# Performance work log

Measured on AMD Instinct MI355X. Metric: run time of the kernel, lower is better.

The kernel has to match this reference:

```python
import jax, jax.numpy as jnp
import numpy as np

B, S_IMG, S_TXT = 1, 3072, 512
D_MODEL, H, D_HEAD = 3072, 24, 128
INNER = H * D_HEAD
EPS = 1e-5


def rms_norm(x, w):
    # x: [..., D_HEAD]
    var = jnp.mean(jnp.square(x), axis=-1, keepdims=True)
    return x * jax.lax.rsqrt(var + EPS) * w


def apply_rope(x, cos, sin):
    # x: [B,S,H,D]; cos/sin: [S,D]; interleaved (non-neox) rotation
    x1 = x[..., 0::2]
    x2 = x[..., 1::2]
    rot = jnp.stack([-x2, x1], axis=-1).reshape(x.shape)
    c = cos[None, :, None, :]
    s = sin[None, :, None, :]
    return x * c + rot * s


def setup_inputs() -> dict:
    key = jax.random.key(0)
    ks = jax.random.split(key, 12)
    sc = 1.0 / np.sqrt(D_MODEL)
    ang = jax.random.uniform(ks[10], (S_TXT + S_IMG, D_HEAD), jnp.float32, 0.0, 2 * np.pi)
    return {
        "hidden_states": jax.random.normal(ks[0], (B, S_IMG, D_MODEL), jnp.float32),
        "encoder_hidden_states": jax.random.normal(ks[1], (B, S_TXT, D_MODEL), jnp.float32),
        "cos": jnp.cos(ang),
        "sin": jnp.sin(ang),
        "W_qkv": jax.random.normal(ks[2], (3 * INNER, D_MODEL), jnp.float32) * sc,
        "W_add_qkv": jax.random.normal(ks[3], (3 * INNER, D_MODEL), jnp.float32) * sc,
        "b_add_qkv": jnp.zeros((3 * INNER,), jnp.float32),
        "norm_q_w": jnp.ones((D_HEAD,), jnp.float32),
        "norm_k_w": jnp.ones((D_HEAD,), jnp.float32),
        "norm_add_q_w": jnp.ones((D_HEAD,), jnp.float32),
        "norm_add_k_w": jnp.ones((D_HEAD,), jnp.float32),
        "W_out": jax.random.normal(ks[4], (D_MODEL, INNER), jnp.float32) * sc,
        "b_out": jnp.zeros((D_MODEL,), jnp.float32),
        "W_add_out": jax.random.normal(ks[5], (D_MODEL, INNER), jnp.float32) * sc,
        "b_add_out": jnp.zeros((D_MODEL,), jnp.float32),
    }


def reference(hidden_states, encoder_hidden_states, cos, sin,
              W_qkv, W_add_qkv, b_add_qkv,
              norm_q_w, norm_k_w, norm_add_q_w, norm_add_k_w,
              W_out, b_out, W_add_out, b_add_out):
    # fused QKV projections
    qkv = jnp.einsum('bsd,ed->bse', hidden_states, W_qkv)
    q, k, v = jnp.split(qkv, 3, axis=-1)
    eqkv = jnp.einsum('bsd,ed->bse', encoder_hidden_states, W_add_qkv) + b_add_qkv
    eq, ek, ev = jnp.split(eqkv, 3, axis=-1)

    def heads(x):
        return x.reshape(x.shape[0], x.shape[1], H, D_HEAD)

    q, k, v = heads(q), heads(k), heads(v)
    eq, ek, ev = heads(eq), heads(ek), heads(ev)

    # per-head RMSNorm on queries/keys
    q = rms_norm(q, norm_q_w)
    k = rms_norm(k, norm_k_w)
    eq = rms_norm(eq, norm_add_q_w)
    ek = rms_norm(ek, norm_add_k_w)

    # joint concat: text first, then image
    q = jnp.concatenate([eq, q], axis=1)
    k = jnp.concatenate([ek, k], axis=1)
    v = jnp.concatenate([ev, v], axis=1)

    # RoPE on full joint sequence
    q = apply_rope(q, cos, sin)
    k = apply_rope(k, cos, sin)

    # non-causal softmax attention, scale = 1/sqrt(head_dim)
    scale = 1.0 / np.sqrt(D_HEAD)
    scores = jnp.einsum('bqhd,bkhd->bhqk', q, k) * scale
    probs = jax.nn.softmax(scores, axis=-1)
    out = jnp.einsum('bhqk,bkhd->bqhd', probs, v)  # [B,S,H,D]
    out = out.reshape(out.shape[0], out.shape[1], INNER)

    enc_out = out[:, :S_TXT]
    img_out = out[:, S_TXT:]
    enc_out = jnp.einsum('bse,de->bsd', enc_out, W_add_out) + b_add_out
    img_out = jnp.einsum('bse,de->bsd', img_out, W_out) + b_out
    return (img_out, enc_out)
```

## Files before the change

### kernel.cpp

```cpp
#include <hip/hip_runtime.h>


typedef unsigned short u16;
typedef __attribute__((ext_vector_type(2))) unsigned short u16x2;
typedef __attribute__((ext_vector_type(4))) unsigned short u16x4;
typedef __attribute__((ext_vector_type(8))) unsigned short u16x8;
typedef __attribute__((ext_vector_type(8))) short bf16x8;
typedef __attribute__((ext_vector_type(4))) float f32x4;
typedef __attribute__((ext_vector_type(16))) float f32x16;
typedef __attribute__((ext_vector_type(4))) unsigned u32x4;

#define DEV __device__ __forceinline__

DEV u16 f2bf(float f) {
  unsigned u = __builtin_bit_cast(unsigned, f);
  u = (u + 0x7FFFu + ((u >> 16) & 1u)) >> 16;
  return (u16)u;
}
DEV float bf2f(u16 s) { return __builtin_bit_cast(float, (unsigned)s << 16); }

DEV void store_out(u16* p, float v)  { *p = f2bf(v); }
DEV void store_out(float* p, float v) { *p = v; }

#define AS1(p) (const __attribute__((address_space(1))) void*)(p)
#define AS3(p) (__attribute__((address_space(3))) void*)(p)
#define GLL16(g, l) __builtin_amdgcn_global_load_lds(AS1(g), AS3(l), 16, 0, 0)

#define BAR() do { asm volatile("" ::: "memory"); __builtin_amdgcn_s_barrier(); \
                   asm volatile("" ::: "memory"); } while (0)
#define VMC8() asm volatile("s_waitcnt vmcnt(8)" ::: "memory")
#define VMC4() asm volatile("s_waitcnt vmcnt(4)" ::: "memory")
#define VMC0() asm volatile("s_waitcnt vmcnt(0)" ::: "memory")

__global__ __launch_bounds__(256) void cvt_kernel(const float* __restrict__ src,
                                                  u16* __restrict__ dst, int n4) {
  int i = blockIdx.x * blockDim.x + threadIdx.x;
  int stride = gridDim.x * blockDim.x;
  for (; i < n4; i += stride) {
    float4 v = reinterpret_cast<const float4*>(src)[i];
    u16x4 o;
    o.x = f2bf(v.x); o.y = f2bf(v.y); o.z = f2bf(v.z); o.w = f2bf(v.w);
    reinterpret_cast<u16x4*>(dst)[i] = o;
  }
}

template <typename OT>
__global__ __launch_bounds__(512, 2) void gemm256(
    const u16* __restrict__ A,
    const u16* __restrict__ Bimg, const u16* __restrict__ Benc,
    const float* __restrict__ biasImg, const float* __restrict__ biasEnc,
    OT* __restrict__ Cimg, OT* __restrict__ Cenc,
    int N, int K, int split, int nwg) {
  const int bid = blockIdx.x;
  const int swz = (bid & 7) * (nwg >> 3) + (bid >> 3);
  const int ntn = N >> 8;
  const int mt = swz / ntn, nt = swz % ntn;
  const int m0 = mt << 8, n0 = nt << 8;
  const u16* B = (m0 < split) ? Benc : Bimg;
  const float* bias = (m0 < split) ? biasEnc : biasImg;

  __shared__ u16 lds[2][2][16384];

  const int tid = threadIdx.x, w = tid >> 6, lane = tid & 63;
  const int wm = w >> 2, wn = w & 3;
  const int q = lane & 15, hi = lane >> 4;
  const size_t ldb = (size_t)K * 2;

  f32x4 acc[8][4];
#pragma unroll
  for (int i = 0; i < 8; ++i)
#pragma unroll
    for (int j = 0; j < 4; ++j)
#pragma unroll
      for (int r = 0; r < 4; ++r) acc[i][j][r] = 0.f;

  auto STAGE = [&](int d, int kt) {
    const char* sA = (const char*)A + (size_t)m0 * ldb + kt * 128;
    const char* sB = (const char*)B + (size_t)n0 * ldb + kt * 128;
    char* dA = (char*)&lds[d][0][0];
    char* dB = (char*)&lds[d][1][0];
#pragma unroll
    for (int j = 0; j < 4; ++j) {
      int base = j * 8192 + w * 1024;
      int off = base + lane * 16;
      int row = off >> 7;
      int src = (off & 127) ^ ((row & 7) << 4);
      GLL16(sA + (size_t)row * ldb + src, dA + base);
      GLL16(sB + (size_t)row * ldb + src, dB + base);
    }
  };
  auto LDA = [&](int d, int i, int ks) -> bf16x8 {
    int row = wm * 128 + i * 16 + q;
    int cb = ks * 64 + hi * 16;
    return *(const bf16x8*)((const char*)&lds[d][0][0] + row * 128 + (cb ^ ((row & 7) << 4)));
  };
  auto LDB = [&](int d, int j, int ks) -> bf16x8 {
    int row = wn * 64 + j * 16 + q;
    int cb = ks * 64 + hi * 16;
    return *(const bf16x8*)((const char*)&lds[d][1][0] + row * 128 + (cb ^ ((row & 7) << 4)));
  };

  auto HALF = [&](int d) {
    bf16x8 bfr[4][2];
#pragma unroll
    for (int ph = 0; ph < 4; ++ph) {
      if (ph == 0) {
#pragma unroll
        for (int j = 0; j < 4; ++j)
#pragma unroll
          for (int ks = 0; ks < 2; ++ks) bfr[j][ks] = LDB(d, j, ks);
      }
      bf16x8 af[2][2];
#pragma unroll
      for (int m = 0; m < 2; ++m)
#pragma unroll
        for (int ks = 0; ks < 2; ++ks) af[m][ks] = LDA(d, 2 * ph + m, ks);
      __builtin_amdgcn_s_setprio(1);
#pragma unroll
      for (int m = 0; m < 2; ++m)
#pragma unroll
        for (int j = 0; j < 4; ++j)
#pragma unroll
          for (int ks = 0; ks < 2; ++ks)
            acc[2 * ph + m][j] = __builtin_amdgcn_mfma_f32_16x16x32_bf16(
                af[m][ks], bfr[j][ks], acc[2 * ph + m][j], 0, 0, 0);
      __builtin_amdgcn_s_setprio(0);
      if (ph < 3) BAR();
    }
  };

  const int NT2 = K >> 7;
  STAGE(0, 0);
  STAGE(1, 1);
  VMC8();
  BAR();
  for (int t = 0; t < NT2; ++t) {
    HALF(0);
    BAR();
    if (t + 1 < NT2) { STAGE(0, 2 * t + 2); VMC8(); }
    else             VMC0();
    BAR();
    HALF(1);
    BAR();
    if (t + 1 < NT2) { STAGE(1, 2 * t + 3); VMC8(); }
    else             VMC0();
    BAR();
  }

#pragma unroll
  for (int i = 0; i < 8; ++i) {
    int rbase = m0 + wm * 128 + i * 16 + (hi << 2);
#pragma unroll
    for (int j = 0; j < 4; ++j) {
      int col = n0 + wn * 64 + j * 16 + q;
      float bv = bias ? bias[col] : 0.f;
#pragma unroll
      for (int r = 0; r < 4; ++r) {
        int row = rbase + r;
        float v = acc[i][j][r] + bv;
        if (row < split) store_out(&Cenc[(size_t)row * N + col], v);
        else             store_out(&Cimg[(size_t)(row - split) * N + col], v);
      }
    }
  }
}

__global__ __launch_bounds__(256) void norm_rope(
    u16* __restrict__ qkv, u16* __restrict__ vt,
    const float* __restrict__ cosT, const float* __restrict__ sinT,
    const float* __restrict__ nqw_img, const float* __restrict__ nkw_img,
    const float* __restrict__ nqw_enc, const float* __restrict__ nkw_enc) {
  const int h = blockIdx.y;
  const int s0 = blockIdx.x * 64;
  const int tid = threadIdx.x, w = tid >> 6, lane = tid & 63;
  const bool enc = (s0 < 512);
  const float* nqw = enc ? nqw_enc : nqw_img;
  const float* nkw = enc ? nkw_enc : nkw_img;
  const float SCL = 0.12751743f;
  const float wq0 = nqw[2 * lane], wq1 = nqw[2 * lane + 1];
  const float wk0 = nkw[2 * lane], wk1 = nkw[2 * lane + 1];
  u16x8 va0, va1, vb0, vb1;
#pragma unroll
  for (int r = 0; r < 16; ++r) {
    const int s = s0 + w * 16 + r;
    const size_t rowb = (size_t)s * 9216 + h * 128 + 2 * lane;
    float2 cv = *(const float2*)&cosT[(size_t)s * 128 + 2 * lane];
    float2 sv = *(const float2*)&sinT[(size_t)s * 128 + 2 * lane];
    {
      u16x2 qu = *(u16x2*)&qkv[rowb];
      float x0 = bf2f(qu.x), x1 = bf2f(qu.y);
      float ss = x0 * x0 + x1 * x1;
#pragma unroll
      for (int d = 1; d < 64; d <<= 1) ss += __shfl_xor(ss, d);
      float rms = rsqrtf(ss * (1.0f / 128.0f) + 1e-5f);
      x0 *= rms * wq0; x1 *= rms * wq1;
      float o0 = (x0 * cv.x - x1 * sv.x) * SCL;
      float o1 = (x1 * cv.y + x0 * sv.y) * SCL;
      u16x2 ou; ou.x = f2bf(o0); ou.y = f2bf(o1);
      *(u16x2*)&qkv[rowb] = ou;
    }
    {
      u16x2 ku = *(u16x2*)&qkv[rowb + 3072];
      float x0 = bf2f(ku.x), x1 = bf2f(ku.y);
      float ss = x0 * x0 + x1 * x1;
#pragma unroll
      for (int d = 1; d < 64; d <<= 1) ss += __shfl_xor(ss, d);
      float rms = rsqrtf(ss * (1.0f / 128.0f) + 1e-5f);
      x0 *= rms * wk0; x1 *= rms * wk1;
      float o0 = x0 * cv.x - x1 * sv.x;
      float o1 = x1 * cv.y + x0 * sv.y;
      u16x2 ou; ou.x = f2bf(o0); ou.y = f2bf(o1);
      *(u16x2*)&qkv[rowb + 3072] = ou;
    }
    {
      u16x2 vu = *(u16x2*)&qkv[rowb + 6144];
      if (r < 8) { va0[r] = vu.x; vb0[r] = vu.y; }
      else       { va1[r - 8] = vu.x; vb1[r - 8] = vu.y; }
    }
  }
  const size_t vbase = (size_t)h * 128 * 3584 + (size_t)(2 * lane) * 3584 + s0 + w * 16;
  *(u16x8*)&vt[vbase]            = va0;
  *(u16x8*)&vt[vbase + 8]        = va1;
  *(u16x8*)&vt[vbase + 3584]     = vb0;
  *(u16x8*)&vt[vbase + 3584 + 8] = vb1;
}

__global__ __launch_bounds__(256, 2) void attn_kernel(
    const u16* __restrict__ qkv, const u16* __restrict__ vt,
    u16* __restrict__ aout) {
  const int bid = blockIdx.x;
  const int qt = bid / 24;
  const int rr = bid % 24;
  const int h = (rr % 8) * 3 + (rr / 8);
  const int tid = threadIdx.x, w = tid >> 6, lane = tid & 63;
  const int q32 = lane & 31, hi5 = lane >> 5;
  const int qbase = qt * 128 + w * 32;
  __shared__ u16 Klds[2][4096];
  __shared__ u16 Vlds[2][4096];

  bf16x8 aq[8];
  {
    const u16* qp = qkv + (size_t)(qbase + q32) * 9216 + h * 128 + hi5 * 8;
#pragma unroll
    for (int ds = 0; ds < 8; ++ds) aq[ds] = *(const bf16x8*)(qp + ds * 16);
  }
  float m_i = -1e30f, l_i = 0.f;
  f32x16 o[4];
#pragma unroll
  for (int dt = 0; dt < 4; ++dt)
#pragma unroll
    for (int r = 0; r < 16; ++r) o[dt][r] = 0.f;
  const size_t vhead = (size_t)h * 128 * 3584;

  auto STAGE_K = [&](int kt0, int b) {
    const char* src = (const char*)(qkv + (size_t)(kt0 + q32) * 9216 + 3072 + h * 128) + hi5 * 16;
    char* dst = (char*)Klds[b] + w * 2048 + lane * 16;
#pragma unroll
    for (int j = 0; j < 2; ++j)
      GLL16(src + (w * 2 + j) * 32, dst + j * 1024);
  };
  auto STAGE_V = [&](int kt0, int b) {
    char* dst = (char*)Vlds[b] + w * 2048 + lane * 16;
#pragma unroll
    for (int j = 0; j < 2; ++j) {
      const int u = w * 2 + j, dt = u >> 1, ks = u & 1;
      GLL16((const char*)(vt + vhead + (size_t)(dt * 32 + q32) * 3584 + kt0) + ks * 32 + hi5 * 16,
            dst + j * 1024);
    }
  };

  auto PACK = [&](const float* p, bf16x8* out2) {
    unsigned w0[4], w1[4];
#pragma unroll
    for (int g = 0; g < 4; ++g) {
      asm("v_cvt_pk_bf16_f32 %0, %1, %2" : "=v"(w0[g]) : "v"(p[4 * g + 0]), "v"(p[4 * g + 1]));
      asm("v_cvt_pk_bf16_f32 %0, %1, %2" : "=v"(w1[g]) : "v"(p[4 * g + 2]), "v"(p[4 * g + 3]));
    }
    asm("v_permlane32_swap_b32 %0, %1" : "+v"(w0[0]), "+v"(w0[1]));
    asm("v_permlane32_swap_b32 %0, %1" : "+v"(w1[0]), "+v"(w1[1]));
    asm("v_permlane32_swap_b32 %0, %1" : "+v"(w0[2]), "+v"(w0[3]));
    asm("v_permlane32_swap_b32 %0, %1" : "+v"(w1[2]), "+v"(w1[3]));
    u32x4 lo = {w0[0], w1[0], w0[1], w1[1]};
    u32x4 hi_ = {w0[2], w1[2], w0[3], w1[3]};
    out2[0] = __builtin_bit_cast(bf16x8, lo);
    out2[1] = __builtin_bit_cast(bf16x8, hi_);
  };

  const int NT = 112;
  STAGE_K(0, 0);   STAGE_V(0, 0);
  STAGE_K(32, 1);  STAGE_V(32, 1);
  for (int t = 0; t < NT; ++t) {
    const int b = t & 1;
    if (t + 1 < NT) VMC4(); else VMC0();
    BAR();

    f32x16 s0;
#pragma unroll
    for (int r = 0; r < 16; ++r) s0[r] = 0.f;
    __builtin_amdgcn_s_setprio(1);
#pragma unroll
    for (int ds = 0; ds < 8; ++ds) {
      bf16x8 k0 = *(const bf16x8*)((const char*)Klds[b] + ds * 1024 + lane * 16);
      s0 = __builtin_amdgcn_mfma_f32_32x32x16_bf16(k0, aq[ds], s0, 0, 0, 0);
    }
    __builtin_amdgcn_s_setprio(0);

    float mx = s0[0];
#pragma unroll
    for (int r = 1; r < 16; ++r) mx = fmaxf(mx, s0[r]);
    mx = fmaxf(mx, __shfl_xor(mx, 32));
    if (!__all(mx - m_i <= 8.f)) {
      float mnew = fmaxf(m_i, mx);
      float alpha = __builtin_amdgcn_exp2f(m_i - mnew);
      m_i = mnew;
      l_i *= alpha;
#pragma unroll
      for (int r = 0; r < 16; ++r) {
        int qr = (r & 3) + 8 * (r >> 2) + 4 * hi5;
        float ar = __shfl(alpha, qr);
#pragma unroll
        for (int dt = 0; dt < 4; ++dt) o[dt][r] *= ar;
      }
    }
    float p0[16];
    float psum = 0.f;
#pragma unroll
    for (int r = 0; r < 16; ++r) { p0[r] = __builtin_amdgcn_exp2f(s0[r] - m_i); psum += p0[r]; }
    psum += __shfl_xor(psum, 32);
    l_i += psum;

    bf16x8 pa[2];
    PACK(p0, pa);

    __builtin_amdgcn_s_setprio(1);
#pragma unroll
    for (int dt = 0; dt < 4; ++dt) {
#pragma unroll
      for (int ks = 0; ks < 2; ++ks) {
        bf16x8 bv = *(const bf16x8*)((const char*)Vlds[b] + (dt * 2 + ks) * 1024 + lane * 16);
        o[dt] = __builtin_amdgcn_mfma_f32_32x32x16_bf16(pa[ks], bv, o[dt], 0, 0, 0);
      }
    }
    __builtin_amdgcn_s_setprio(0);
    BAR();
    if (t + 2 < NT) { STAGE_K((t + 2) * 32, b); STAGE_V((t + 2) * 32, b); }
  }

#pragma unroll
  for (int r = 0; r < 16; ++r) {
    const int qr = (r & 3) + 8 * (r >> 2) + 4 * hi5;
    const float lr = __shfl(l_i, qr);
    const float inv = 1.0f / lr;
    const size_t srow = (size_t)(qbase + qr) * 3072 + h * 128 + q32;
#pragma unroll
    for (int dt = 0; dt < 4; ++dt)
      aout[srow + dt * 32] = f2bf(o[dt][r] * inv);
  }
}

extern "C" void kernel_launch(void* const* d_in, const int* in_sizes, int n_in,
                              void* d_out, int out_size, void* d_ws, size_t ws_size,
                              hipStream_t stream) {
  (void)in_sizes; (void)n_in; (void)out_size; (void)ws_size;
  const float* hs    = (const float*)d_in[0];
  const float* ehs   = (const float*)d_in[1];
  const float* cosT  = (const float*)d_in[2];
  const float* sinT  = (const float*)d_in[3];
  const float* Wqkv  = (const float*)d_in[4];
  const float* Wadd  = (const float*)d_in[5];
  const float* bAdd  = (const float*)d_in[6];
  const float* nqw   = (const float*)d_in[7];
  const float* nkw   = (const float*)d_in[8];
  const float* naqw  = (const float*)d_in[9];
  const float* nakw  = (const float*)d_in[10];
  const float* Wout  = (const float*)d_in[11];
  const float* bout  = (const float*)d_in[12];
  const float* Waddo = (const float*)d_in[13];
  const float* baddo = (const float*)d_in[14];

  char* ws = (char*)d_ws;
  u16* Ain = (u16*)(ws);
  u16* WqI = (u16*)(ws + 22020096);
  u16* WqE = WqI + (size_t)9216 * 3072;
  u16* WoI = (u16*)(ws + 135266304);
  u16* WoE = WoI + (size_t)3072 * 3072;
  u16* qkv = (u16*)(ws + 173015040);
  u16* vt   = Ain;
  u16* aout = WqI;

  cvt_kernel<<<1024, 256, 0, stream>>>(ehs,   Ain,                      512 * 3072 / 4);
  cvt_kernel<<<1024, 256, 0, stream>>>(hs,    Ain + (size_t)512 * 3072, 3072 * 3072 / 4);
  cvt_kernel<<<2048, 256, 0, stream>>>(Wqkv,  WqI, 9216 * 3072 / 4);
  cvt_kernel<<<2048, 256, 0, stream>>>(Wadd,  WqE, 9216 * 3072 / 4);
  cvt_kernel<<<1024, 256, 0, stream>>>(Wout,  WoI, 3072 * 3072 / 4);
  cvt_kernel<<<1024, 256, 0, stream>>>(Waddo, WoE, 3072 * 3072 / 4);

  gemm256<u16><<<dim3(504), 512, 0, stream>>>(Ain, WqI, WqE, nullptr, bAdd,
                                              qkv + (size_t)512 * 9216, qkv, 9216, 3072, 512, 504);
  norm_rope<<<dim3(56, 24), 256, 0, stream>>>(qkv, vt, cosT, sinT, nqw, nkw, naqw, nakw);
  attn_kernel<<<dim3(672), 256, 0, stream>>>(qkv, vt, aout);
  float* outp = (float*)d_out;
  gemm256<float><<<dim3(168), 512, 0, stream>>>(aout, WoI, WoE, bout, baddo,
                                                outp, outp + (size_t)3072 * 3072, 3072, 3072, 512, 168);
}
```

Baseline: 642.0 us.

## Switch GEMM to triple-buffered K=32 stages with MFMA-fragment LDS layout and 2D tile swizzle

Restructures the 256x256 bf16 GEMM main loop from double-buffered 64-wide K tiles to three 32-wide K stages in LDS, which puts more loads in flight ahead of compute. Global-to-LDS copies now write data directly in per-lane MFMA fragment order, so LDS reads become contiguous with no XOR swizzle. The workgroup-to-tile mapping becomes a fixed 2x4 grouping of tiles across the 8 XCD slots to improve L2 reuse. The trade-offs are more loop iterations with barriers per K, and a tile mapping hardcoded to 7 M-tiles per group, which only fits these problem sizes.

After: 702.1 us. 9.4% more time.

```diff
diff --git a/kernel.cpp b/kernel.cpp
--- a/kernel.cpp
+++ b/kernel.cpp
@@ -50,16 +50,18 @@
     const u16* __restrict__ Bimg, const u16* __restrict__ Benc,
     const float* __restrict__ biasImg, const float* __restrict__ biasEnc,
     OT* __restrict__ Cimg, OT* __restrict__ Cenc,
-    int N, int K, int split, int nwg) {
+    int N, int K, int split) {
   const int bid = blockIdx.x;
-  const int swz = (bid & 7) * (nwg >> 3) + (bid >> 3);
   const int ntn = N >> 8;
-  const int mt = swz / ntn, nt = swz % ntn;
+  const int CN = ntn >> 2;
+  const int x = bid & 7, i5 = bid >> 3;
+  const int mt = (x >> 2) * 7 + i5 / CN;
+  const int nt = (x & 3) * CN + i5 % CN;
   const int m0 = mt << 8, n0 = nt << 8;
   const u16* B = (m0 < split) ? Benc : Bimg;
   const float* bias = (m0 < split) ? biasEnc : biasImg;
 
-  __shared__ u16 lds[2][2][16384];
+  __shared__ u16 lds[3][2][8192];
 
   const int tid = threadIdx.x, w = tid >> 6, lane = tid & 63;
   const int wm = w >> 2, wn = w & 3;
@@ -74,77 +76,60 @@
 #pragma unroll
       for (int r = 0; r < 4; ++r) acc[i][j][r] = 0.f;
 
-  auto STAGE = [&](int d, int kt) {
-    const char* sA = (const char*)A + (size_t)m0 * ldb + kt * 128;
-    const char* sB = (const char*)B + (size_t)n0 * ldb + kt * 128;
-    char* dA = (char*)&lds[d][0][0];
-    char* dB = (char*)&lds[d][1][0];
-#pragma unroll
-    for (int j = 0; j < 4; ++j) {
-      int base = j * 8192 + w * 1024;
-      int off = base + lane * 16;
-      int row = off >> 7;
-      int src = (off & 127) ^ ((row & 7) << 4);
-      GLL16(sA + (size_t)row * ldb + src, dA + base);
-      GLL16(sB + (size_t)row * ldb + src, dB + base);
-    }
-  };
-  auto LDA = [&](int d, int i, int ks) -> bf16x8 {
-    int row = wm * 128 + i * 16 + q;
-    int cb = ks * 64 + hi * 16;
-    return *(const bf16x8*)((const char*)&lds[d][0][0] + row * 128 + (cb ^ ((row & 7) << 4)));
-  };
-  auto LDB = [&](int d, int j, int ks) -> bf16x8 {
-    int row = wn * 64 + j * 16 + q;
-    int cb = ks * 64 + hi * 16;
-    return *(const bf16x8*)((const char*)&lds[d][1][0] + row * 128 + (cb ^ ((row & 7) << 4)));
-  };
-
-  auto HALF = [&](int d) {
-    bf16x8 bfr[4][2];
-#pragma unroll
-    for (int ph = 0; ph < 4; ++ph) {
-      if (ph == 0) {
-#pragma unroll
-        for (int j = 0; j < 4; ++j)
-#pragma unroll
-          for (int ks = 0; ks < 2; ++ks) bfr[j][ks] = LDB(d, j, ks);
-      }
-      bf16x8 af[2][2];
-#pragma unroll
-      for (int m = 0; m < 2; ++m)
-#pragma unroll
-        for (int ks = 0; ks < 2; ++ks) af[m][ks] = LDA(d, 2 * ph + m, ks);
-      __builtin_amdgcn_s_setprio(1);
-#pragma unroll
-      for (int m = 0; m < 2; ++m)
-#pragma unroll
-        for (int j = 0; j < 4; ++j)
-#pragma unroll
-          for (int ks = 0; ks < 2; ++ks)
-            acc[2 * ph + m][j] = __builtin_amdgcn_mfma_f32_16x16x32_bf16(
-                af[m][ks], bfr[j][ks], acc[2 * ph + m][j], 0, 0, 0);
-      __builtin_amdgcn_s_setprio(0);
-      if (ph < 3) BAR();
-    }
-  };
-
-  const int NT2 = K >> 7;
-  STAGE(0, 0);
-  STAGE(1, 1);
+  auto STAGE = [&](int b, int kt) {
+    const char* sA = (const char*)A + (size_t)m0 * ldb + (size_t)kt * 64;
+    const char* sB = (const char*)B + (size_t)n0 * ldb + (size_t)kt * 64;
+    char* dA = (char*)&lds[b][0][0];
+    char* dB = (char*)&lds[b][1][0];
+#pragma unroll
+    for (int g = 0; g < 2; ++g) {
+      const int u = g * 8 + w;
+      const size_t so = (size_t)(u * 16 + q) * ldb + hi * 16;
+      GLL16(sA + so, dA + u * 1024 + lane * 16);
+      GLL16(sB + so, dB + u * 1024 + lane * 16);
+    }
+  };
+  auto LDA = [&](int b, int i) -> bf16x8 {
+    return *(const bf16x8*)((const char*)&lds[b][0][0] + (wm * 8 + i) * 1024 + lane * 16);
+  };
+  auto LDB = [&](int b, int j) -> bf16x8 {
+    return *(const bf16x8*)((const char*)&lds[b][1][0] + (wn * 4 + j) * 1024 + lane * 16);
+  };
+
+  const int NT = K >> 5;
+  STAGE(0, 0); STAGE(1, 1); STAGE(2, 2);
   VMC8();
   BAR();
-  for (int t = 0; t < NT2; ++t) {
-    HALF(0);
+  int b = 0;
+  for (int t = 0; t < NT; ++t) {
+    bf16x8 bfr[4];
+#pragma unroll
+    for (int j = 0; j < 4; ++j) bfr[j] = LDB(b, j);
+    bf16x8 af[4];
+#pragma unroll
+    for (int i = 0; i < 4; ++i) af[i] = LDA(b, i);
+    __builtin_amdgcn_s_setprio(1);
+#pragma unroll
+    for (int i = 0; i < 4; ++i)
+#pragma unroll
+      for (int j = 0; j < 4; ++j)
+        acc[i][j] = __builtin_amdgcn_mfma_f32_16x16x32_bf16(af[i], bfr[j], acc[i][j], 0, 0, 0);
+    __builtin_amdgcn_s_setprio(0);
+#pragma unroll
+    for (int i = 0; i < 4; ++i) af[i] = LDA(b, i + 4);
+    __builtin_amdgcn_s_setprio(1);
+#pragma unroll
+    for (int i = 0; i < 4; ++i)
+#pragma unroll
+      for (int j = 0; j < 4; ++j)
+        acc[i + 4][j] = __builtin_amdgcn_mfma_f32_16x16x32_bf16(af[i], bfr[j], acc[i + 4][j], 0, 0, 0);
+    __builtin_amdgcn_s_setprio(0);
     BAR();
-    if (t + 1 < NT2) { STAGE(0, 2 * t + 2); VMC8(); }
-    else             VMC0();
+    if (t + 3 < NT)      { STAGE(b, t + 3); VMC8(); }
+    else if (t + 2 < NT) VMC4();
+    else if (t + 1 < NT) VMC0();
     BAR();
-    HALF(1);
-    BAR();
-    if (t + 1 < NT2) { STAGE(1, 2 * t + 3); VMC8(); }
-    else             VMC0();
-    BAR();
+    b = (b == 2) ? 0 : b + 1;
   }
 
 #pragma unroll
@@ -396,10 +381,10 @@
   cvt_kernel<<<1024, 256, 0, stream>>>(Waddo, WoE, 3072 * 3072 / 4);
 
   gemm256<u16><<<dim3(504), 512, 0, stream>>>(Ain, WqI, WqE, nullptr, bAdd,
-                                              qkv + (size_t)512 * 9216, qkv, 9216, 3072, 512, 504);
+                                              qkv + (size_t)512 * 9216, qkv, 9216, 3072, 512);
   norm_rope<<<dim3(56, 24), 256, 0, stream>>>(qkv, vt, cosT, sinT, nqw, nkw, naqw, nakw);
   attn_kernel<<<dim3(672), 256, 0, stream>>>(qkv, vt, aout);
   float* outp = (float*)d_out;
   gemm256<float><<<dim3(168), 512, 0, stream>>>(aout, WoI, WoE, bout, baddo,
-                                                outp, outp + (size_t)3072 * 3072, 3072, 3072, 512, 168);
-}
+                                                outp, outp + (size_t)3072 * 3072, 3072, 3072, 512);
+}
```
